# Optimization experiments

Hardware: AMD Instinct MI355X
Metric: run time of the kernel (lower is better)

The kernel has to match this reference:

```python
import jax, jax.numpy as jnp
import numpy as np

B, T, D_IN, E, H = 2, 2048, 1024, 64, 16  # batch, num_tokens, input dim, emb_size(per-head), num_heads


def setup_inputs() -> dict:
    key = jax.random.key(0)
    ks = jax.random.split(key, 6)
    s = 0.02
    inp = jax.random.normal(ks[0], (B, T, D_IN), dtype=jnp.float32)
    # causal mask: 1.0 where attention is disallowed (j > i), matching `scaled_compat -= mask * 1e9`
    mask = jnp.triu(jnp.ones((T, T), dtype=jnp.float32), k=1)
    Wq = jax.random.normal(ks[1], (D_IN, E * H), dtype=jnp.float32) * s
    Wk = jax.random.normal(ks[2], (D_IN, E * H), dtype=jnp.float32) * s
    Wv = jax.random.normal(ks[3], (D_IN, E * H), dtype=jnp.float32) * s
    Wu = jax.random.normal(ks[4], (E * H, E), dtype=jnp.float32) * s
    bu = jnp.zeros((E,), dtype=jnp.float32)
    return {"inp": inp, "mask": mask, "Wq": Wq, "Wk": Wk, "Wv": Wv, "Wu": Wu, "bu": bu}


def reference(inp, mask, Wq, Wk, Wv, Wu, bu):
    b = inp.shape[0]
    q = inp @ Wq  # [B,T,E*H]
    k = inp @ Wk
    v = inp @ Wv
    # NOTE: original reshapes last dim as (E, H) -> heads on fastest axis (interleaved layout)
    q = q.reshape(b, T, E, H)
    k = k.reshape(b, T, E, H)
    v = v.reshape(b, T, E, H)
    scores = jnp.einsum("bteh,bseh->bhts", q, k) / jnp.sqrt(jnp.float32(E))  # [B,H,T,T]
    if mask is not None:
        scores = scores - mask * 1e9
    attn = jax.nn.softmax(scores, axis=-1)
    wv = jnp.einsum("bhts,bseh->bhte", attn, v)  # [B,H,T,E]
    # transpose [0,2,3,1] -> [B,T,E,H], then flatten to [B,T,E*H] (H fastest, matching original)
    wv = jnp.transpose(wv, (0, 2, 3, 1)).reshape(b, T, E * H)
    return wv @ Wu + bu  # unify Dense(emb_size), with bias
```

## Files before the change

kernel.cpp:

```cpp
#include <hip/hip_runtime.h>


typedef __bf16 bf16x8 __attribute__((ext_vector_type(8)));
typedef __bf16 bf16x4 __attribute__((ext_vector_type(4)));
typedef float f32x4 __attribute__((ext_vector_type(4)));
typedef unsigned short u16;
typedef unsigned int u32;

#define AS1 __attribute__((address_space(1)))
#define AS3 __attribute__((address_space(3)))

__device__ __forceinline__ void gll16(const void* g, void* l) {
    __builtin_amdgcn_global_load_lds((const AS1 u32*)g, (AS3 u32*)l, 16, 0, 0);
}

__device__ __forceinline__ u16 f2bf(float f) {
    __bf16 h = (__bf16)f;
    union { __bf16 h; u16 u; } v; v.h = h; return v.u;
}

#define MM 4096
#define SCALE_LOG2E 0.18033688011112042f

__global__ void prep(const float* __restrict__ in, u16* __restrict__ out,
                     const float* __restrict__ Wq, const float* __restrict__ Wk,
                     const float* __restrict__ Wv, const float* __restrict__ Wu,
                     u16* __restrict__ wqt, u16* __restrict__ wkt,
                     u16* __restrict__ wvt, u16* __restrict__ wut) {
    __shared__ float lds[32][33];
    int bid = blockIdx.x, tid = threadIdx.x;
    if (bid < 4096) {
        int i = bid * 256 + tid;
        float4 f = ((const float4*)in)[i];
        bf16x4 o;
        o[0] = (__bf16)f.x; o[1] = (__bf16)f.y; o[2] = (__bf16)f.z; o[3] = (__bf16)f.w;
        ((bf16x4*)out)[i] = o;
        return;
    }
    int bid2 = bid - 4096;
    int z = bid2 >> 10, y = (bid2 >> 5) & 31, x = bid2 & 31;
    const float* src; u16* dst; int N;
    if (z == 0)      { src = Wq; dst = wqt; N = 1024; }
    else if (z == 1) { src = Wk; dst = wkt; N = 1024; }
    else if (z == 2) { src = Wv; dst = wvt; N = 1024; }
    else             { src = Wu; dst = wut; N = 64; if (y >= 2) return; }
    int k0 = x * 32, n0 = y * 32;
    int c = tid & 31, r0 = tid >> 5;
#pragma unroll
    for (int p = 0; p < 4; ++p) {
        int r = r0 + p * 8;
        lds[r][c] = src[(k0 + r) * N + n0 + c];
    }
    __syncthreads();
#pragma unroll
    for (int p = 0; p < 4; ++p) {
        int n = n0 + r0 + p * 8;
        if (z < 3) {
            int rnew = ((n & 15) << 6) | (n >> 4);
            dst[rnew * 1024 + k0 + c] = f2bf(lds[c][n - n0]);
        } else {
            int k = k0 + c;
            int kp = ((k & 15) << 6) | (k >> 4);
            dst[n * 1024 + kp] = f2bf(lds[c][n - n0]);
        }
    }
}

__global__ __launch_bounds__(256) void gemm_qkv(const u16* __restrict__ xb,
                                                const u16* __restrict__ wqt,
                                                const u16* __restrict__ wkt,
                                                const u16* __restrict__ wvt,
                                                u16* __restrict__ qh, u16* __restrict__ kh,
                                                u16* __restrict__ vh) {
    int z = blockIdx.z;
    const u16* wt = (z == 0) ? wqt : (z == 1) ? wkt : wvt;
    u16* dst      = (z == 0) ? qh  : (z == 1) ? kh  : vh;
    __shared__ u16 lA[3][128 * 32];
    __shared__ u16 lB[3][128 * 32];
    int tid = threadIdx.x;
    int m0 = blockIdx.x * 128, n0 = blockIdx.y * 128;
    int lane = tid & 63, w = tid >> 6;
    int wr = w >> 1, wc = w & 1;
    int l15 = lane & 15, quad = lane >> 4;
    f32x4 acc[4][4] = {};
    int srow = tid >> 2;
    int scolx = ((tid & 3) * 8) ^ (((srow >> 1) & 3) << 3);
    const int qsw = (quad ^ ((l15 >> 1) & 3)) * 8;
    const u16* ga = xb + (m0 + srow) * 1024 + scolx;
    const u16* gb = wt + (n0 + srow) * 1024 + scolx;
#pragma unroll
    for (int t0 = 0; t0 < 2; ++t0)
#pragma unroll
        for (int pp = 0; pp < 2; ++pp) {
            gll16(ga + pp * 65536 + t0 * 32, lA[t0] + (pp * 256 + tid) * 8);
            gll16(gb + pp * 65536 + t0 * 32, lB[t0] + (pp * 256 + tid) * 8);
        }
    int cur = 0;
#pragma unroll 1
    for (int kk = 0; kk < 32; ++kk) {
        if (kk < 31) asm volatile("s_waitcnt vmcnt(4)" ::: "memory");
        else         asm volatile("s_waitcnt vmcnt(0)" ::: "memory");
        __builtin_amdgcn_s_barrier();
        if (kk + 2 < 32) {
            int nxt = cur + 2; if (nxt >= 3) nxt -= 3;
            int kb = (kk + 2) * 32;
#pragma unroll
            for (int pp = 0; pp < 2; ++pp) {
                gll16(ga + pp * 65536 + kb, lA[nxt] + (pp * 256 + tid) * 8);
                gll16(gb + pp * 65536 + kb, lB[nxt] + (pp * 256 + tid) * 8);
            }
        }
        bf16x8 af[4], bfr[4];
#pragma unroll
        for (int i = 0; i < 4; ++i)
            af[i] = *(const bf16x8*)(lA[cur] + (wr * 64 + i * 16 + l15) * 32 + qsw);
#pragma unroll
        for (int j = 0; j < 4; ++j)
            bfr[j] = *(const bf16x8*)(lB[cur] + (wc * 64 + j * 16 + l15) * 32 + qsw);
#pragma unroll
        for (int i = 0; i < 4; ++i)
#pragma unroll
            for (int j = 0; j < 4; ++j)
                acc[i][j] = __builtin_amdgcn_mfma_f32_16x16x32_bf16(af[i], bfr[j], acc[i][j], 0, 0, 0);
        ++cur; if (cur == 3) cur = 0;
    }
    int bb = m0 >> 11;
    int hb = (n0 >> 6) + wc;
    if (z < 2) {
        float scale = (z == 0) ? SCALE_LOG2E : 1.f;
#pragma unroll
        for (int i = 0; i < 4; ++i)
#pragma unroll
            for (int r = 0; r < 4; ++r) {
                int m = m0 + wr * 64 + i * 16 + quad * 4 + r;
                bf16x4 o;
                o[0] = (__bf16)(acc[i][0][r] * scale); o[1] = (__bf16)(acc[i][1][r] * scale);
                o[2] = (__bf16)(acc[i][2][r] * scale); o[3] = (__bf16)(acc[i][3][r] * scale);
                *(bf16x4*)(dst + m * 1024 + hb * 64 + l15 * 4) = o;
            }
    } else {
#pragma unroll
        for (int j = 0; j < 4; ++j)
#pragma unroll
            for (int r = 0; r < 4; ++r) {
                bf16x4 o;
                o[0] = (__bf16)acc[0][j][r]; o[1] = (__bf16)acc[1][j][r];
                o[2] = (__bf16)acc[2][j][r]; o[3] = (__bf16)acc[3][j][r];
                *(bf16x4*)(dst + (((bb * 16 + hb) * 64) + j * 16 + l15) * 2048 +
                           (m0 & 2047) + wr * 64 + (quad * 4 + r) * 4) = o;
            }
    }
}

__global__ __launch_bounds__(256) void attn(const u16* __restrict__ qh, const u16* __restrict__ kh,
                                            const u16* __restrict__ vh, u16* __restrict__ ot,
                                            float* __restrict__ part, float* __restrict__ lp) {
    __shared__ u16 smem[25600];
    u16* sPQ = smem;
    const int tid = threadIdx.x;
    const int lane = tid & 63, w = tid >> 6;
    const int quad = lane >> 4, l15 = lane & 15;
    const int s = blockIdx.x, by = blockIdx.y;
    int qt, j0, j1, half;
    if (s < 8)       { qt = 7 - s;  j0 = 0;      j1 = 2 * qt + 2; half = -1; }
    else if (s < 16) { qt = s;      j0 = 0;      j1 = qt + 1;     half = 0;  }
    else             { qt = s - 8;  j0 = qt + 1; j1 = 2 * qt + 2; half = 1;  }
    const int b = by >> 4, h = by & 15;
    const int row0 = tid >> 3;
    const int cb0 = (tid & 7) ^ (row0 & 7);
    const u16* kg0 = kh + (b * 2048) * 1024 + h * 64 + row0 * 1024 + cb0 * 8;
    const u16* vg0 = vh + (by * 64) * 2048 + row0 * 2048 + cb0 * 8;
    const int fsw = (l15 & 7) * 8;

    const u16* qg = qh + (b * 2048 + qt * 128) * 1024 + h * 64;
#pragma unroll
    for (int p = 0; p < 4; ++p) {
        int c = p * 256 + tid;
        gll16(qg + (c >> 3) * 1024 + (c & 7) * 8, sPQ + c * 8);
    }
    __syncthreads();
    bf16x8 aq[2][2];
#pragma unroll
    for (int rg = 0; rg < 2; ++rg)
#pragma unroll
        for (int k2 = 0; k2 < 2; ++k2)
            aq[rg][k2] = *(const bf16x8*)(sPQ + (w * 32 + rg * 16 + l15) * 64 + k2 * 32 + quad * 8);

    {
        u16* sK0 = smem + 9216;
        u16* sV0 = smem + 17408;
        gll16(kg0 + j0 * 65536,         sK0 + tid * 8);
        gll16(kg0 + j0 * 65536 + 32768, sK0 + (256 + tid) * 8);
        gll16(vg0 + j0 * 64,            sV0 + tid * 8);
        gll16(vg0 + j0 * 64 + 65536,    sV0 + (256 + tid) * 8);
    }
    float lpart[2][4] = {};
    f32x4 oacc[2][4] = {};
    u16* sPw = sPQ + w * 2304;
    for (int jt = j0; jt < j1; ++jt) {
        int cur = (jt - j0) & 1;
        u16* sK = smem + 9216 + cur * 4096;
        u16* sV = smem + 17408 + cur * 4096;
        asm volatile("s_waitcnt vmcnt(0)" ::: "memory");
        __builtin_amdgcn_s_barrier();
        if (jt + 1 < j1) {
            u16* sKn = smem + 9216 + (cur ^ 1) * 4096;
            u16* sVn = smem + 17408 + (cur ^ 1) * 4096;
            gll16(kg0 + (jt + 1) * 65536,         sKn + tid * 8);
            gll16(kg0 + (jt + 1) * 65536 + 32768, sKn + (256 + tid) * 8);
            gll16(vg0 + (jt + 1) * 64,            sVn + tid * 8);
            gll16(vg0 + (jt + 1) * 64 + 65536,    sVn + (256 + tid) * 8);
        }
        f32x4 sacc[2][4] = {};
        __builtin_amdgcn_s_setprio(1);
#pragma unroll
        for (int j4 = 0; j4 < 4; ++j4)
#pragma unroll
            for (int k2 = 0; k2 < 2; ++k2) {
                bf16x8 bk = *(const bf16x8*)(sK + (j4 * 16 + l15) * 64 + (((k2 * 4 + quad) * 8) ^ fsw));
                sacc[0][j4] = __builtin_amdgcn_mfma_f32_16x16x32_bf16(aq[0][k2], bk, sacc[0][j4], 0, 0, 0);
                sacc[1][j4] = __builtin_amdgcn_mfma_f32_16x16x32_bf16(aq[1][k2], bk, sacc[1][j4], 0, 0, 0);
            }
        __builtin_amdgcn_s_setprio(0);
        if (jt >= 2 * qt) {
            int soff = (jt - 2 * qt) * 64;
#pragma unroll
            for (int rg = 0; rg < 2; ++rg)
#pragma unroll
                for (int j4 = 0; j4 < 4; ++j4)
#pragma unroll
                    for (int r = 0; r < 4; ++r) {
                        int sg = soff + j4 * 16 + l15;
                        int tg = w * 32 + rg * 16 + quad * 4 + r;
                        if (sg > tg) sacc[rg][j4][r] = -1e30f;
                    }
        }
#pragma unroll
        for (int rg = 0; rg < 2; ++rg)
#pragma unroll
            for (int r = 0; r < 4; ++r) {
                float p0 = __builtin_amdgcn_exp2f(sacc[rg][0][r]);
                float p1 = __builtin_amdgcn_exp2f(sacc[rg][1][r]);
                float p2 = __builtin_amdgcn_exp2f(sacc[rg][2][r]);
                float p3 = __builtin_amdgcn_exp2f(sacc[rg][3][r]);
                lpart[rg][r] += (p0 + p1) + (p2 + p3);
                bf16x4 o;
                o[0] = (__bf16)p0; o[1] = (__bf16)p1; o[2] = (__bf16)p2; o[3] = (__bf16)p3;
                *(bf16x4*)(sPw + (rg * 16 + quad * 4 + r) * 72 + l15 * 4) = o;
            }
        bf16x8 ap[2][2];
#pragma unroll
        for (int rg = 0; rg < 2; ++rg)
#pragma unroll
            for (int k2 = 0; k2 < 2; ++k2)
                ap[rg][k2] = *(const bf16x8*)(sPw + (rg * 16 + l15) * 72 + k2 * 32 + quad * 8);
        __builtin_amdgcn_s_setprio(1);
#pragma unroll
        for (int e4 = 0; e4 < 4; ++e4)
#pragma unroll
            for (int k2 = 0; k2 < 2; ++k2) {
                bf16x8 bv = *(const bf16x8*)(sV + (e4 * 16 + l15) * 64 + (((k2 * 4 + quad) * 8) ^ fsw));
                oacc[0][e4] = __builtin_amdgcn_mfma_f32_16x16x32_bf16(ap[0][k2], bv, oacc[0][e4], 0, 0, 0);
                oacc[1][e4] = __builtin_amdgcn_mfma_f32_16x16x32_bf16(ap[1][k2], bv, oacc[1][e4], 0, 0, 0);
            }
        __builtin_amdgcn_s_setprio(0);
    }
    if (half < 0) {
#pragma unroll
        for (int rg = 0; rg < 2; ++rg)
#pragma unroll
            for (int r = 0; r < 4; ++r) {
                float rs = lpart[rg][r];
#pragma unroll
                for (int off = 1; off < 16; off <<= 1) rs += __shfl_xor(rs, off, 16);
                float inv = 1.f / rs;
                int t = qt * 128 + w * 32 + rg * 16 + quad * 4 + r;
                int base = (b * 2048 + t) * 1024 + h * 64;
#pragma unroll
                for (int e4 = 0; e4 < 4; ++e4)
                    ot[base + e4 * 16 + l15] = f2bf(oacc[rg][e4][r] * inv);
            }
    } else {
        int pb = by * 8 + (qt - 8);
        float* pg = part + (pb * 2 + half) * 8192;
        float* lg = lp + pb * 256 + half * 128;
#pragma unroll
        for (int rg = 0; rg < 2; ++rg)
#pragma unroll
            for (int r = 0; r < 4; ++r) {
                float rs = lpart[rg][r];
#pragma unroll
                for (int off = 1; off < 16; off <<= 1) rs += __shfl_xor(rs, off, 16);
                int row = w * 32 + rg * 16 + quad * 4 + r;
                if (l15 == 0) lg[row] = rs;
#pragma unroll
                for (int e4 = 0; e4 < 4; ++e4)
                    pg[row * 64 + e4 * 16 + l15] = oacc[rg][e4][r];
            }
    }
}

__global__ __launch_bounds__(256) void gemm_out(const u16* __restrict__ ot,
                                                const float* __restrict__ part,
                                                const float* __restrict__ lp,
                                                const u16* __restrict__ wut,
                                                const float* __restrict__ bu, float* __restrict__ out) {
    __shared__ float red[4][1088];
    int tid = threadIdx.x, lane = tid & 63, w = tid >> 6;
    int quad = lane >> 4, l15 = lane & 15;
    int m0 = blockIdx.x * 16;
    int b = m0 >> 11, t0 = m0 & 2047, qt = t0 >> 7;
    f32x4 acc[4] = {};
    const u16* bptr = wut + l15 * 1024 + w * 256 + quad * 8;
    if (qt < 8) {
        const u16* aptr = ot + (m0 + l15) * 1024 + w * 256 + quad * 8;
#pragma unroll
        for (int kk = 0; kk < 8; ++kk) {
            bf16x8 af = *(const bf16x8*)(aptr + kk * 32);
#pragma unroll
            for (int j = 0; j < 4; ++j) {
                bf16x8 bfr = *(const bf16x8*)(bptr + j * 16 * 1024 + kk * 32);
                acc[j] = __builtin_amdgcn_mfma_f32_16x16x32_bf16(af, bfr, acc[j], 0, 0, 0);
            }
        }
    } else {
        int rowp = (t0 & 127) + l15;
        float inv4[4];
#pragma unroll
        for (int hh = 0; hh < 4; ++hh) {
            int pb = (b * 16 + w * 4 + hh) * 8 + (qt - 8);
            inv4[hh] = 1.f / (lp[pb * 256 + rowp] + lp[pb * 256 + 128 + rowp]);
        }
#pragma unroll
        for (int kk = 0; kk < 8; ++kk) {
            const int hh = kk >> 1;
            int pb = (b * 16 + w * 4 + hh) * 8 + (qt - 8);
            int e = (kk & 1) * 32 + quad * 8;
            const float* pA = part + pb * 16384 + rowp * 64 + e;
            float4 a0 = *(const float4*)(pA);
            float4 a1 = *(const float4*)(pA + 4);
            float4 c0 = *(const float4*)(pA + 8192);
            float4 c1 = *(const float4*)(pA + 8192 + 4);
            float inv = inv4[hh];
            bf16x8 af;
            af[0] = (__bf16)((a0.x + c0.x) * inv); af[1] = (__bf16)((a0.y + c0.y) * inv);
            af[2] = (__bf16)((a0.z + c0.z) * inv); af[3] = (__bf16)((a0.w + c0.w) * inv);
            af[4] = (__bf16)((a1.x + c1.x) * inv); af[5] = (__bf16)((a1.y + c1.y) * inv);
            af[6] = (__bf16)((a1.z + c1.z) * inv); af[7] = (__bf16)((a1.w + c1.w) * inv);
#pragma unroll
            for (int j = 0; j < 4; ++j) {
                bf16x8 bfr = *(const bf16x8*)(bptr + j * 16 * 1024 + kk * 32);
                acc[j] = __builtin_amdgcn_mfma_f32_16x16x32_bf16(af, bfr, acc[j], 0, 0, 0);
            }
        }
    }
#pragma unroll
    for (int j = 0; j < 4; ++j)
#pragma unroll
        for (int r = 0; r < 4; ++r)
            red[w][(j * 16 + l15) * 17 + quad * 4 + r] = acc[j][r];
    __syncthreads();
    int n = tid & 63, mq = tid >> 6;
    float bias = bu[n];
#pragma unroll
    for (int i = 0; i < 4; ++i) {
        int m = mq * 4 + i;
        float s = red[0][n * 17 + m] + red[1][n * 17 + m] + red[2][n * 17 + m] + red[3][n * 17 + m];
        out[(m0 + m) * 64 + n] = s + bias;
    }
}

#define OFF_XB   0u
#define OFF_WQT  8388608u
#define OFF_WKT  10485760u
#define OFF_WVT  12582912u
#define OFF_WUT  14680064u
#define OFF_QH   14811136u
#define OFF_KH   23199744u
#define OFF_VH   31588352u
#define OFF_OT   OFF_XB
#define OFF_PART 39976960u
#define OFF_LP   56754176u

extern "C" void kernel_launch(void* const* d_in, const int* in_sizes, int n_in,
                              void* d_out, int out_size, void* d_ws, size_t ws_size,
                              hipStream_t stream) {
    (void)in_sizes; (void)n_in; (void)out_size; (void)ws_size;
    const float* inp = (const float*)d_in[0];
    const float* Wq = (const float*)d_in[2];
    const float* Wk = (const float*)d_in[3];
    const float* Wv = (const float*)d_in[4];
    const float* Wu = (const float*)d_in[5];
    const float* bu = (const float*)d_in[6];
    float* out = (float*)d_out;
    char* ws = (char*)d_ws;
    u16* xb  = (u16*)(ws + OFF_XB);
    u16* wqt = (u16*)(ws + OFF_WQT);
    u16* wkt = (u16*)(ws + OFF_WKT);
    u16* wvt = (u16*)(ws + OFF_WVT);
    u16* wut = (u16*)(ws + OFF_WUT);
    u16* qh  = (u16*)(ws + OFF_QH);
    u16* kh  = (u16*)(ws + OFF_KH);
    u16* vh  = (u16*)(ws + OFF_VH);
    u16* ot  = (u16*)(ws + OFF_OT);
    float* part = (float*)(ws + OFF_PART);
    float* lpw  = (float*)(ws + OFF_LP);

    prep<<<8192, 256, 0, stream>>>(inp, xb, Wq, Wk, Wv, Wu, wqt, wkt, wvt, wut);
    gemm_qkv<<<dim3(32, 8, 3), 256, 0, stream>>>(xb, wqt, wkt, wvt, qh, kh, vh);
    attn<<<dim3(24, 32), 256, 0, stream>>>(qh, kh, vh, ot, part, lpw);
    gemm_out<<<256, 256, 0, stream>>>(ot, part, lpw, wut, bu, out);
}
```

Before: 161.4 us.

## Triple-buffer K/V tiles in attention and drop LDS swizzle in QKV GEMM

The attention kernel moves from double to triple buffering of the K/V tiles. It prefetches two tiles ahead and waits with vmcnt(4) instead of draining all loads each iteration, which should hide global-load latency better. LDS grows from about 51KB to 67KB, which may cut occupancy. Separately, the QKV GEMM drops the XOR swizzle on its LDS tile layout, which simplifies addressing but can bring back LDS bank conflicts on the fragment reads.

```diff
diff --git a/kernel.cpp b/kernel.cpp
--- a/kernel.cpp
+++ b/kernel.cpp
@@ -83,11 +83,9 @@
     int wr = w >> 1, wc = w & 1;
     int l15 = lane & 15, quad = lane >> 4;
     f32x4 acc[4][4] = {};
-    int srow = tid >> 2;
-    int scolx = ((tid & 3) * 8) ^ (((srow >> 1) & 3) << 3);
-    const int qsw = (quad ^ ((l15 >> 1) & 3)) * 8;
-    const u16* ga = xb + (m0 + srow) * 1024 + scolx;
-    const u16* gb = wt + (n0 + srow) * 1024 + scolx;
+    int srow = tid >> 2, scol = (tid & 3) * 8;
+    const u16* ga = xb + (m0 + srow) * 1024 + scol;
+    const u16* gb = wt + (n0 + srow) * 1024 + scol;
 #pragma unroll
     for (int t0 = 0; t0 < 2; ++t0)
 #pragma unroll
@@ -113,10 +111,10 @@
         bf16x8 af[4], bfr[4];
 #pragma unroll
         for (int i = 0; i < 4; ++i)
-            af[i] = *(const bf16x8*)(lA[cur] + (wr * 64 + i * 16 + l15) * 32 + qsw);
+            af[i] = *(const bf16x8*)(lA[cur] + (wr * 64 + i * 16 + l15) * 32 + quad * 8);
 #pragma unroll
         for (int j = 0; j < 4; ++j)
-            bfr[j] = *(const bf16x8*)(lB[cur] + (wc * 64 + j * 16 + l15) * 32 + qsw);
+            bfr[j] = *(const bf16x8*)(lB[cur] + (wc * 64 + j * 16 + l15) * 32 + quad * 8);
 #pragma unroll
         for (int i = 0; i < 4; ++i)
 #pragma unroll
@@ -155,7 +153,7 @@
 __global__ __launch_bounds__(256) void attn(const u16* __restrict__ qh, const u16* __restrict__ kh,
                                             const u16* __restrict__ vh, u16* __restrict__ ot,
                                             float* __restrict__ part, float* __restrict__ lp) {
-    __shared__ u16 smem[25600];
+    __shared__ u16 smem[33792];
     u16* sPQ = smem;
     const int tid = threadIdx.x;
     const int lane = tid & 63, w = tid >> 6;
@@ -188,28 +186,38 @@
 
     {
         u16* sK0 = smem + 9216;
-        u16* sV0 = smem + 17408;
+        u16* sV0 = smem + 21504;
         gll16(kg0 + j0 * 65536,         sK0 + tid * 8);
         gll16(kg0 + j0 * 65536 + 32768, sK0 + (256 + tid) * 8);
         gll16(vg0 + j0 * 64,            sV0 + tid * 8);
         gll16(vg0 + j0 * 64 + 65536,    sV0 + (256 + tid) * 8);
+        if (j0 + 1 < j1) {
+            u16* sK1 = sK0 + 4096;
+            u16* sV1 = sV0 + 4096;
+            gll16(kg0 + (j0 + 1) * 65536,         sK1 + tid * 8);
+            gll16(kg0 + (j0 + 1) * 65536 + 32768, sK1 + (256 + tid) * 8);
+            gll16(vg0 + (j0 + 1) * 64,            sV1 + tid * 8);
+            gll16(vg0 + (j0 + 1) * 64 + 65536,    sV1 + (256 + tid) * 8);
+        }
     }
     float lpart[2][4] = {};
     f32x4 oacc[2][4] = {};
     u16* sPw = sPQ + w * 2304;
+    int cur = 0;
     for (int jt = j0; jt < j1; ++jt) {
-        int cur = (jt - j0) & 1;
         u16* sK = smem + 9216 + cur * 4096;
-        u16* sV = smem + 17408 + cur * 4096;
-        asm volatile("s_waitcnt vmcnt(0)" ::: "memory");
+        u16* sV = smem + 21504 + cur * 4096;
+        if (jt + 1 < j1) asm volatile("s_waitcnt vmcnt(4)" ::: "memory");
+        else             asm volatile("s_waitcnt vmcnt(0)" ::: "memory");
         __builtin_amdgcn_s_barrier();
-        if (jt + 1 < j1) {
-            u16* sKn = smem + 9216 + (cur ^ 1) * 4096;
-            u16* sVn = smem + 17408 + (cur ^ 1) * 4096;
-            gll16(kg0 + (jt + 1) * 65536,         sKn + tid * 8);
-            gll16(kg0 + (jt + 1) * 65536 + 32768, sKn + (256 + tid) * 8);
-            gll16(vg0 + (jt + 1) * 64,            sVn + tid * 8);
-            gll16(vg0 + (jt + 1) * 64 + 65536,    sVn + (256 + tid) * 8);
+        if (jt + 2 < j1) {
+            int nxt = cur + 2; if (nxt >= 3) nxt -= 3;
+            u16* sKn = smem + 9216 + nxt * 4096;
+            u16* sVn = smem + 21504 + nxt * 4096;
+            gll16(kg0 + (jt + 2) * 65536,         sKn + tid * 8);
+            gll16(kg0 + (jt + 2) * 65536 + 32768, sKn + (256 + tid) * 8);
+            gll16(vg0 + (jt + 2) * 64,            sVn + tid * 8);
+            gll16(vg0 + (jt + 2) * 64 + 65536,    sVn + (256 + tid) * 8);
         }
         f32x4 sacc[2][4] = {};
         __builtin_amdgcn_s_setprio(1);
@@ -264,6 +272,7 @@
                 oacc[1][e4] = __builtin_amdgcn_mfma_f32_16x16x32_bf16(ap[1][k2], bv, oacc[1][e4], 0, 0, 0);
             }
         __builtin_amdgcn_s_setprio(0);
+        ++cur; if (cur == 3) cur = 0;
     }
     if (half < 0) {
 #pragma unroll
```

After: 172.1 us. 1.07x slower.
